# Kernel optimization log

Hardware: AMD Instinct MI355X
Metric: run time of the kernel (lower is better)

The kernel has to match this reference:

```python
import jax, jax.numpy as jnp
import numpy as np

B, C, H, W = 16, 64, 1024, 16  # requires C*W == H per the module's implicit view/matmul constraint
C8 = C // 8


def setup_inputs() -> dict:
    key = jax.random.key(0)
    ks = jax.random.split(key, 7)
    s_in = 1.0 / np.sqrt(C)
    return {
        "x": jax.random.normal(ks[0], (B, C, H, W), dtype=jnp.float32),
        "Wq": jax.random.normal(ks[1], (C8, C), dtype=jnp.float32) * s_in,
        "bq": jax.random.normal(ks[2], (C8,), dtype=jnp.float32) * 0.01,
        "Wk": jax.random.normal(ks[3], (C8, C), dtype=jnp.float32) * s_in,
        "bk": jax.random.normal(ks[4], (C8,), dtype=jnp.float32) * 0.01,
        "Wv": jax.random.normal(ks[5], (C, C), dtype=jnp.float32) * s_in,
        "bv": jax.random.normal(ks[6], (C,), dtype=jnp.float32) * 0.01,
    }


def conv1x1(x, w, b):
    # 1x1 conv == per-pixel channel mixing: [B,C,H,W] x [O,C] -> [B,O,H,W]
    return jnp.einsum("bchw,oc->bohw", x, w) + b[None, :, None, None]


def reference(x, Wq, bq, Wk, bk, Wv, bv):
    b, c, h, w = x.shape
    q = conv1x1(x, Wq, bq)  # [B, C/8, H, W]
    k = conv1x1(x, Wk, bk)  # [B, C/8, H, W]
    v = conv1x1(x, Wv, bv)  # [B, C, H, W]
    # Faithful to torch .view(B, -1, H): row-major reshape, NOT a transpose.
    qf = jnp.swapaxes(q.reshape(b, -1, h), 1, 2)  # [B, H, C8*W]
    kf = k.reshape(b, -1, h)                      # [B, C8*W, H]
    vf = v.reshape(b, -1, h)                      # [B, C*W, H] (C*W == H)
    scores = jax.nn.softmax(jnp.matmul(qf, kf), axis=-1)  # [B, H, H]
    attended = jnp.matmul(scores, vf)             # [B, H, H]
    attended = attended.reshape(v.shape)          # [B, C, H, W]
    return x + attended
```

## Files before the change

### kernel.cpp

```cpp
#include <hip/hip_runtime.h>
#include <stdint.h>

typedef uint32_t u32;
typedef __attribute__((ext_vector_type(4))) float f32x4;
typedef __attribute__((ext_vector_type(8))) short short8;

#define NBATCH 16
#define NPIX   16384
#define NPB    1048576

__device__ __forceinline__ ushort f2bf(float f) {
  u32 b = __builtin_bit_cast(u32, f);
  return (ushort)((b + 0x7FFFu + ((b >> 16) & 1u)) >> 16);
}
__device__ __forceinline__ float bf2f(ushort h) {
  return __builtin_bit_cast(float, (u32)h << 16);
}

__device__ __forceinline__ void gload16(const void* g, void* l) {
  __builtin_amdgcn_global_load_lds(
      (const __attribute__((address_space(1))) u32*)g,
      (__attribute__((address_space(3))) u32*)l,
      16, 0, 0);
}

__global__ void prep_w(const float* __restrict__ Wq, const float* __restrict__ bq,
                       const float* __restrict__ Wk, const float* __restrict__ bk,
                       const float* __restrict__ Wv, const float* __restrict__ bv,
                       float* __restrict__ wp2, float* __restrict__ bpk)
{
  int gid = blockIdx.x * 256 + threadIdx.x;
  if (gid < 5120) {
    int ch = gid / 80;
    int o = gid - ch * 80;
    float v = (o < 8) ? Wq[o * 64 + ch]
            : (o < 16) ? Wk[(o - 8) * 64 + ch]
                       : Wv[(o - 16) * 64 + ch];
    wp2[gid] = v;
  } else if (gid < 5200) {
    int o = gid - 5120;
    bpk[o] = (o < 8) ? bq[o] : (o < 16 ? bk[o - 8] : bv[o - 16]);
  }
}

__global__ __launch_bounds__(320) void proj9(
    const float* __restrict__ x, const float* __restrict__ wp2,
    const float* __restrict__ bpk,
    ushort* __restrict__ Qt2, ushort* __restrict__ Kt2,
    ushort* __restrict__ Vt)
{
  __shared__ __align__(16) char smem[32768];
  float* xs = (float*)smem;
  int t = threadIdx.x;
  int w = t >> 6, lane = t & 63;

  int g = blockIdx.x;
  int lin = (g & 7) * 256 + (g >> 3);
  int b = lin >> 7;
  int l0 = (lin & 127) << 3;
  const float* xb = x + (size_t)b * NPB + l0;

  #pragma unroll
  for (int it = 0; it < 7; ++it) {
    int f0 = (it * 5 + w) * 64;
    if (f0 < 2048) {
      int f = f0 + lane;
      int ch = f >> 5, r2 = f & 31, tc = r2 >> 1, half = r2 & 1;
      gload16(xb + (size_t)ch * NPIX + tc * 1024 + half * 4, xs + f0 * 4);
    }
  }
  __syncthreads();

  int ob = __builtin_amdgcn_readfirstlane(w * 16);
  float acc[16][2];
  #pragma unroll
  for (int o = 0; o < 16; ++o) { float bb = bpk[ob + o]; acc[o][0] = bb; acc[o][1] = bb; }

  for (int ch = 0; ch < 64; ++ch) {
    float2 xv = *(const float2*)&xs[ch * 128 + 2 * lane];
    const float* wr = wp2 + ch * 80 + ob;
    #pragma unroll
    for (int o = 0; o < 16; ++o) {
      float wo = wr[o];
      acc[o][0] += wo * xv.x;
      acc[o][1] += wo * xv.y;
    }
  }
  __syncthreads();

  float*  qkl = (float*)smem;
  ushort* vl  = (ushort*)(smem + 16 * 132 * 4);

  if (w == 0) {
    #pragma unroll
    for (int o = 0; o < 16; ++o) {
      qkl[o * 132 + 2 * lane]     = acc[o][0];
      qkl[o * 132 + 2 * lane + 1] = acc[o][1];
    }
  } else {
    int cb = ob - 16;
    #pragma unroll
    for (int o = 0; o < 16; ++o) {
      u32 pk2 = (u32)f2bf(acc[o][0]) | ((u32)f2bf(acc[o][1]) << 16);
      *(u32*)&vl[(cb + o) * 136 + 2 * lane] = pk2;
    }
  }
  __syncthreads();

  if (t < 128) {
    int l = t >> 4, tcc = t & 15;
    size_t lrow = (size_t)b * 1024 + l0 + l;
    int px = tcc * 8 + l;

    union { ushort s[8]; uint4 v; } qh, ql, kh, kl;
    #pragma unroll
    for (int o = 0; o < 8; ++o) {
      float qv = qkl[o * 132 + px];
      ushort h = f2bf(qv);
      qh.s[o] = h; ql.s[o] = f2bf(qv - bf2f(h));
      float kv = qkl[(8 + o) * 132 + px];
      h = f2bf(kv);
      kh.s[o] = h; kl.s[o] = f2bf(kv - bf2f(h));
    }
    ushort* qrow = Qt2 + lrow * 384 + tcc * 8;
    *(uint4*)qrow         = qh.v;
    *(uint4*)(qrow + 128) = ql.v;
    *(uint4*)(qrow + 256) = qh.v;
    ushort* krow = Kt2 + lrow * 384 + tcc * 8;
    *(uint4*)krow         = kh.v;
    *(uint4*)(krow + 128) = kh.v;
    *(uint4*)(krow + 256) = kl.v;

    ushort* vrow = Vt + lrow * 1024;
    #pragma unroll
    for (int it = 0; it < 4; ++it) {
      int c2 = (it << 4) + tcc;
      union { ushort s[16]; uint4 q[2]; } ov;
      #pragma unroll
      for (int tt = 0; tt < 16; ++tt)
        ov.s[tt] = vl[c2 * 136 + tt * 8 + l];
      *(uint4*)(vrow + c2 * 16)     = ov.q[0];
      *(uint4*)(vrow + c2 * 16 + 8) = ov.q[1];
    }
  }
}

template<int KTOT, bool ADDX>
__global__ __launch_bounds__(256) void gemm_nt(
    const ushort* __restrict__ A, int lda,
    const ushort* __restrict__ B, int ldb,
    float* __restrict__ C, const float* __restrict__ X)
{
  __shared__ ushort Asm[128 * 64];
  __shared__ ushort Bsm[128 * 64];
  int t = threadIdx.x;

  int g = blockIdx.x;
  int lin = (g & 7) * 128 + (g >> 3);
  int bz = lin >> 6;
  int by = (lin >> 3) & 7;
  int bx = lin & 7;
  int m0 = by << 7, n0 = bx << 7;

  const ushort* Ab = A + (size_t)bz * 1024 * lda;
  const ushort* Bb = B + (size_t)bz * 1024 * ldb;
  int wid = t >> 6, lane = t & 63;
  int wm = wid >> 1, wn = wid & 1;

  int swc = (t & 7) ^ ((t >> 3) & 7);
  const ushort* pa = Ab + (size_t)(m0 + (t >> 3)) * lda + swc * 8;
  const ushort* pb = Bb + (size_t)(n0 + (t >> 3)) * ldb + swc * 8;
  ushort* la0 = Asm + (size_t)(t >> 6) * 512;
  ushort* lb0 = Bsm + (size_t)(t >> 6) * 512;

  f32x4 acc[4][4] = {};

  for (int k0 = 0; k0 < KTOT; k0 += 64) {
    __syncthreads();
    #pragma unroll
    for (int i = 0; i < 4; ++i)
      gload16(pa + (size_t)i * 32 * lda + k0, la0 + i * 2048);
    #pragma unroll
    for (int i = 0; i < 4; ++i)
      gload16(pb + (size_t)i * 32 * ldb + k0, lb0 + i * 2048);
    __syncthreads();
    #pragma unroll
    for (int kk = 0; kk < 2; ++kk) {
      short8 af[4], bfr[4];
      #pragma unroll
      for (int mi = 0; mi < 4; ++mi) {
        int rr = (wm << 6) + (mi << 4) + (lane & 15);
        af[mi] = __builtin_bit_cast(short8,
            ((const uint4*)Asm)[rr * 8 + ((kk * 4 + (lane >> 4)) ^ (rr & 7))]);
      }
      #pragma unroll
      for (int ni = 0; ni < 4; ++ni) {
        int rr = (wn << 6) + (ni << 4) + (lane & 15);
        bfr[ni] = __builtin_bit_cast(short8,
            ((const uint4*)Bsm)[rr * 8 + ((kk * 4 + (lane >> 4)) ^ (rr & 7))]);
      }
      #pragma unroll
      for (int mi = 0; mi < 4; ++mi)
        #pragma unroll
        for (int ni = 0; ni < 4; ++ni)
          acc[mi][ni] = __builtin_amdgcn_mfma_f32_16x16x32_bf16(
              af[mi], bfr[ni], acc[mi][ni], 0, 0, 0);
    }
  }

  #pragma unroll
  for (int mi = 0; mi < 4; ++mi) {
    int rbase = m0 + (wm << 6) + (mi << 4) + ((lane >> 4) << 2);
    #pragma unroll
    for (int ni = 0; ni < 4; ++ni) {
      int col = n0 + (wn << 6) + (ni << 4) + (lane & 15);
      f32x4 v = acc[mi][ni];
      #pragma unroll
      for (int rr = 0; rr < 4; ++rr) {
        size_t idx = ((size_t)bz * 1024 + rbase + rr) * 1024 + col;
        if (ADDX) C[idx] = v[rr] + X[idx];
        else      C[idx] = v[rr];
      }
    }
  }
}

__global__ __launch_bounds__(256) void softmax_rows(float* __restrict__ S)
{
  size_t rowi = blockIdx.x;
  float* srow = S + rowi * 1024;
  int t = threadIdx.x;
  float4 v = ((const float4*)srow)[t];
  float m = fmaxf(fmaxf(v.x, v.y), fmaxf(v.z, v.w));
  #pragma unroll
  for (int off = 32; off > 0; off >>= 1) m = fmaxf(m, __shfl_xor(m, off));
  __shared__ float red[8];
  int wid = t >> 6, lane = t & 63;
  if (lane == 0) red[wid] = m;
  __syncthreads();
  m = fmaxf(fmaxf(red[0], red[1]), fmaxf(red[2], red[3]));
  float e0 = __expf(v.x - m), e1 = __expf(v.y - m);
  float e2 = __expf(v.z - m), e3 = __expf(v.w - m);
  float s = e0 + e1 + e2 + e3;
  #pragma unroll
  for (int off = 32; off > 0; off >>= 1) s += __shfl_xor(s, off);
  if (lane == 0) red[4 + wid] = s;
  __syncthreads();
  s = red[4] + red[5] + red[6] + red[7];
  float inv = 1.0f / s;
  union { ushort h[4]; uint2 q; } pk;
  pk.h[0] = f2bf(e0 * inv); pk.h[1] = f2bf(e1 * inv);
  pk.h[2] = f2bf(e2 * inv); pk.h[3] = f2bf(e3 * inv);
  ((uint2*)srow)[t] = pk.q;
}

extern "C" void kernel_launch(void* const* d_in, const int* in_sizes, int n_in,
                              void* d_out, int out_size, void* d_ws, size_t ws_size,
                              hipStream_t stream) {
  const float* x  = (const float*)d_in[0];
  const float* Wq = (const float*)d_in[1];
  const float* bq = (const float*)d_in[2];
  const float* Wk = (const float*)d_in[3];
  const float* bk = (const float*)d_in[4];
  const float* Wv = (const float*)d_in[5];
  const float* bv = (const float*)d_in[6];
  float* out = (float*)d_out;

  char* wsb = (char*)d_ws;
  ushort* Qt2 = (ushort*)wsb;
  ushort* Kt2 = (ushort*)(wsb + 12582912);
  ushort* Vt  = (ushort*)(wsb + 25165824);
  float*  S   = (float*)(wsb + 58720256);
  float*  wp2 = (float*)(wsb + 92274688);
  float*  bpk = wp2 + 5120;

  prep_w<<<21, 256, 0, stream>>>(Wq, bq, Wk, bk, Wv, bv, wp2, bpk);
  proj9<<<2048, 320, 0, stream>>>(x, wp2, bpk, Qt2, Kt2, Vt);
  gemm_nt<384, false><<<1024, 256, 0, stream>>>(Qt2, 384, Kt2, 384, S, nullptr);
  softmax_rows<<<16384, 256, 0, stream>>>(S);
  gemm_nt<1024, true><<<1024, 256, 0, stream>>>((const ushort*)S, 2048, Vt, 1024, out, x);
}
```

Measured before the change: 145.8 us.

## Move 1x1-conv projection to bf16 MFMA with split-precision Q/K

The projection kernel's scalar FP32 FMA loop over 64 channels is replaced by bf16 MFMA 16x16x32 instructions. The weights are pre-packed into bf16 hi/lo fragments. Q/K use hi*hi + hi*lo + lo*hi products to keep near-FP32 accuracy, while V uses a single bf16 product. Block size drops from 320 to 256 threads, and the x tile is truncated to bf16 hi/lo in registers. This cuts ALU time in the projection, at the cost of a small precision change and extra packing work.

```diff
diff --git a/kernel.cpp b/kernel.cpp
--- a/kernel.cpp
+++ b/kernel.cpp
@@ -24,27 +24,36 @@
       16, 0, 0);
 }
 
-__global__ void prep_w(const float* __restrict__ Wq, const float* __restrict__ bq,
-                       const float* __restrict__ Wk, const float* __restrict__ bk,
-                       const float* __restrict__ Wv, const float* __restrict__ bv,
-                       float* __restrict__ wp2, float* __restrict__ bpk)
+__global__ void prep_w2(const float* __restrict__ Wq, const float* __restrict__ bq,
+                        const float* __restrict__ Wk, const float* __restrict__ bk,
+                        const float* __restrict__ Wv, const float* __restrict__ bv,
+                        ushort* __restrict__ Wpk, float* __restrict__ bpk)
 {
   int gid = blockIdx.x * 256 + threadIdx.x;
-  if (gid < 5120) {
-    int ch = gid / 80;
-    int o = gid - ch * 80;
-    float v = (o < 8) ? Wq[o * 64 + ch]
-            : (o < 16) ? Wk[(o - 8) * 64 + ch]
-                       : Wv[(o - 16) * 64 + ch];
-    wp2[gid] = v;
-  } else if (gid < 5200) {
-    int o = gid - 5120;
+  if (gid < 12288) {
+    int m = gid >> 7, kk = gid & 127;
+    int ch = kk & 63;
+    ushort outv = 0;
+    if (m < 8) {
+      float wv = Wq[m * 64 + ch];
+      ushort h = f2bf(wv);
+      outv = (kk < 64) ? h : f2bf(wv - bf2f(h));
+    } else if (m < 16) {
+      float wv = Wk[(m - 8) * 64 + ch];
+      ushort h = f2bf(wv);
+      outv = (kk < 64) ? h : f2bf(wv - bf2f(h));
+    } else if (m < 80) {
+      outv = (kk < 64) ? f2bf(Wv[(m - 16) * 64 + ch]) : (ushort)0;
+    }
+    Wpk[gid] = outv;
+  } else if (gid < 12368) {
+    int o = gid - 12288;
     bpk[o] = (o < 8) ? bq[o] : (o < 16 ? bk[o - 8] : bv[o - 16]);
   }
 }
 
-__global__ __launch_bounds__(320) void proj9(
-    const float* __restrict__ x, const float* __restrict__ wp2,
+__global__ __launch_bounds__(256) void proj10(
+    const float* __restrict__ x, const ushort* __restrict__ Wpk,
     const float* __restrict__ bpk,
     ushort* __restrict__ Qt2, ushort* __restrict__ Kt2,
     ushort* __restrict__ Vt)
@@ -53,6 +62,7 @@
   float* xs = (float*)smem;
   int t = threadIdx.x;
   int w = t >> 6, lane = t & 63;
+  int l15 = lane & 15, l4 = lane >> 4;
 
   int g = blockIdx.x;
   int lin = (g & 7) * 256 + (g >> 3);
@@ -61,49 +71,97 @@
   const float* xb = x + (size_t)b * NPB + l0;
 
   #pragma unroll
-  for (int it = 0; it < 7; ++it) {
-    int f0 = (it * 5 + w) * 64;
-    if (f0 < 2048) {
-      int f = f0 + lane;
-      int ch = f >> 5, r2 = f & 31, tc = r2 >> 1, half = r2 & 1;
-      gload16(xb + (size_t)ch * NPIX + tc * 1024 + half * 4, xs + f0 * 4);
-    }
-  }
-  __syncthreads();
-
-  int ob = __builtin_amdgcn_readfirstlane(w * 16);
-  float acc[16][2];
-  #pragma unroll
-  for (int o = 0; o < 16; ++o) { float bb = bpk[ob + o]; acc[o][0] = bb; acc[o][1] = bb; }
-
-  for (int ch = 0; ch < 64; ++ch) {
-    float2 xv = *(const float2*)&xs[ch * 128 + 2 * lane];
-    const float* wr = wp2 + ch * 80 + ob;
-    #pragma unroll
-    for (int o = 0; o < 16; ++o) {
-      float wo = wr[o];
-      acc[o][0] += wo * xv.x;
-      acc[o][1] += wo * xv.y;
+  for (int it = 0; it < 8; ++it) {
+    int f0 = (it * 4 + w) * 64;
+    int f = f0 + lane;
+    int ch = f >> 5, r2 = f & 31, tc = r2 >> 1, half = r2 & 1;
+    gload16(xb + (size_t)ch * NPIX + tc * 1024 + half * 4, xs + f0 * 4);
+  }
+
+  const uint4* Wp4 = (const uint4*)Wpk;
+  uint4 Afrag[12];
+  #pragma unroll
+  for (int kc = 0; kc < 4; ++kc)
+    Afrag[kc] = Wp4[l15 * 16 + kc * 4 + l4];
+  #pragma unroll
+  for (int mt = 1; mt < 5; ++mt)
+    #pragma unroll
+    for (int kc = 0; kc < 2; ++kc)
+      Afrag[2 + mt * 2 + kc] = Wp4[(mt * 16 + l15) * 16 + kc * 4 + l4];
+
+  f32x4 acc[5][2];
+  #pragma unroll
+  for (int mt = 0; mt < 5; ++mt) {
+    f32x4 bv4;
+    #pragma unroll
+    for (int r = 0; r < 4; ++r) bv4[r] = bpk[mt * 16 + l4 * 4 + r];
+    acc[mt][0] = bv4; acc[mt][1] = bv4;
+  }
+
+  __syncthreads();
+
+  #pragma unroll
+  for (int i = 0; i < 2; ++i) {
+    int px = (w * 2 + i) * 16 + l15;
+    u32 xr[16];
+    #pragma unroll
+    for (int kc = 0; kc < 2; ++kc)
+      #pragma unroll
+      for (int j = 0; j < 8; ++j)
+        xr[kc * 8 + j] = ((const u32*)xs)[(kc * 32 + l4 * 8 + j) * 128 + px];
+    uint4 bxh[2], bxl[2];
+    #pragma unroll
+    for (int kc = 0; kc < 2; ++kc)
+      #pragma unroll
+      for (int p = 0; p < 4; ++p) {
+        u32 a = xr[kc * 8 + 2 * p], c = xr[kc * 8 + 2 * p + 1];
+        ((u32*)&bxh[kc])[p] = (a >> 16) | (c & 0xFFFF0000u);
+        float fa = __builtin_bit_cast(float, a) -
+                   __builtin_bit_cast(float, a & 0xFFFF0000u);
+        float fc = __builtin_bit_cast(float, c) -
+                   __builtin_bit_cast(float, c & 0xFFFF0000u);
+        u32 la = __builtin_bit_cast(u32, fa), lc = __builtin_bit_cast(u32, fc);
+        ((u32*)&bxl[kc])[p] = (la >> 16) | (lc & 0xFFFF0000u);
+      }
+    short8 h0 = __builtin_bit_cast(short8, bxh[0]);
+    short8 h1 = __builtin_bit_cast(short8, bxh[1]);
+    short8 s0 = __builtin_bit_cast(short8, bxl[0]);
+    short8 s1 = __builtin_bit_cast(short8, bxl[1]);
+    acc[0][i] = __builtin_amdgcn_mfma_f32_16x16x32_bf16(
+        __builtin_bit_cast(short8, Afrag[0]), h0, acc[0][i], 0, 0, 0);
+    acc[0][i] = __builtin_amdgcn_mfma_f32_16x16x32_bf16(
+        __builtin_bit_cast(short8, Afrag[1]), h1, acc[0][i], 0, 0, 0);
+    acc[0][i] = __builtin_amdgcn_mfma_f32_16x16x32_bf16(
+        __builtin_bit_cast(short8, Afrag[0]), s0, acc[0][i], 0, 0, 0);
+    acc[0][i] = __builtin_amdgcn_mfma_f32_16x16x32_bf16(
+        __builtin_bit_cast(short8, Afrag[1]), s1, acc[0][i], 0, 0, 0);
+    acc[0][i] = __builtin_amdgcn_mfma_f32_16x16x32_bf16(
+        __builtin_bit_cast(short8, Afrag[2]), h0, acc[0][i], 0, 0, 0);
+    acc[0][i] = __builtin_amdgcn_mfma_f32_16x16x32_bf16(
+        __builtin_bit_cast(short8, Afrag[3]), h1, acc[0][i], 0, 0, 0);
+    #pragma unroll
+    for (int mt = 1; mt < 5; ++mt) {
+      acc[mt][i] = __builtin_amdgcn_mfma_f32_16x16x32_bf16(
+          __builtin_bit_cast(short8, Afrag[2 + mt * 2]), h0, acc[mt][i], 0, 0, 0);
+      acc[mt][i] = __builtin_amdgcn_mfma_f32_16x16x32_bf16(
+          __builtin_bit_cast(short8, Afrag[3 + mt * 2]), h1, acc[mt][i], 0, 0, 0);
     }
   }
   __syncthreads();
 
   float*  qkl = (float*)smem;
   ushort* vl  = (ushort*)(smem + 16 * 132 * 4);
-
-  if (w == 0) {
-    #pragma unroll
-    for (int o = 0; o < 16; ++o) {
-      qkl[o * 132 + 2 * lane]     = acc[o][0];
-      qkl[o * 132 + 2 * lane + 1] = acc[o][1];
-    }
-  } else {
-    int cb = ob - 16;
-    #pragma unroll
-    for (int o = 0; o < 16; ++o) {
-      u32 pk2 = (u32)f2bf(acc[o][0]) | ((u32)f2bf(acc[o][1]) << 16);
-      *(u32*)&vl[(cb + o) * 136 + 2 * lane] = pk2;
-    }
+  #pragma unroll
+  for (int i = 0; i < 2; ++i) {
+    int px = (w * 2 + i) * 16 + l15;
+    #pragma unroll
+    for (int r = 0; r < 4; ++r)
+      qkl[(l4 * 4 + r) * 132 + px] = acc[0][i][r];
+    #pragma unroll
+    for (int mt = 1; mt < 5; ++mt)
+      #pragma unroll
+      for (int r = 0; r < 4; ++r)
+        vl[((mt - 1) * 16 + l4 * 4 + r) * 136 + px] = f2bf(acc[mt][i][r]);
   }
   __syncthreads();
 
@@ -271,11 +329,11 @@
   ushort* Kt2 = (ushort*)(wsb + 12582912);
   ushort* Vt  = (ushort*)(wsb + 25165824);
   float*  S   = (float*)(wsb + 58720256);
-  float*  wp2 = (float*)(wsb + 92274688);
-  float*  bpk = wp2 + 5120;
-
-  prep_w<<<21, 256, 0, stream>>>(Wq, bq, Wk, bk, Wv, bv, wp2, bpk);
-  proj9<<<2048, 320, 0, stream>>>(x, wp2, bpk, Qt2, Kt2, Vt);
+  ushort* Wpk = (ushort*)(wsb + 92274688);
+  float*  bpk = (float*)(wsb + 92274688 + 24576);
+
+  prep_w2<<<49, 256, 0, stream>>>(Wq, bq, Wk, bk, Wv, bv, Wpk, bpk);
+  proj10<<<2048, 256, 0, stream>>>(x, Wpk, bpk, Qt2, Kt2, Vt);
   gemm_nt<384, false><<<1024, 256, 0, stream>>>(Qt2, 384, Kt2, 384, S, nullptr);
   softmax_rows<<<16384, 256, 0, stream>>>(S);
   gemm_nt<1024, true><<<1024, 256, 0, stream>>>((const ushort*)S, 2048, Vt, 1024, out, x);
```

Result: faster. 129.7 us (-11.0%).
